# Performance work log

Hardware: AMD Instinct MI355X
Metric: run time of the kernel (lower is better)

The kernel has to match this reference:

```python
import jax, jax.numpy as jnp
import numpy as np

B, T = 32, 1024
VOCAB, E, H, K = 50000, 256, 512, 48
HD = H // 2
NEG = -10000.0


def setup_inputs() -> dict:
    key = jax.random.key(0)
    ks = jax.random.split(key, 8)
    n = lambda k, sh, sc: jax.random.normal(k, sh, jnp.float32) * sc
    return {
        "sentence": jax.random.randint(ks[0], (B, T), 0, VOCAB, dtype=jnp.int32),
        "embedding": n(ks[1], (VOCAB, E), 0.02),
        "Wih_f": n(ks[2], (4 * HD, E), 0.05), "Whh_f": n(ks[3], (4 * HD, HD), 0.05),
        "bih_f": jnp.zeros((4 * HD,), jnp.float32), "bhh_f": jnp.zeros((4 * HD,), jnp.float32),
        "Wih_b": n(ks[4], (4 * HD, E), 0.05), "Whh_b": n(ks[5], (4 * HD, HD), 0.05),
        "bih_b": jnp.zeros((4 * HD,), jnp.float32), "bhh_b": jnp.zeros((4 * HD,), jnp.float32),
        "W_out": n(ks[6], (K, H), 0.05), "b_out": jnp.zeros((K,), jnp.float32),
        "transitions": n(ks[7], (K, K), 1.0),
    }


def _lstm_dir(x, Wih, Whh, bih, bhh, reverse):
    # x: [T,B,E]; PyTorch gate order i,f,g,o
    h0 = jnp.zeros((x.shape[1], Whh.shape[1]), x.dtype)

    def step(carry, xt):
        h, c = carry
        g = xt @ Wih.T + bih + h @ Whh.T + bhh
        i, f, gg, o = jnp.split(g, 4, axis=-1)
        c = jax.nn.sigmoid(f) * c + jax.nn.sigmoid(i) * jnp.tanh(gg)
        h = jax.nn.sigmoid(o) * jnp.tanh(c)
        return (h, c), h

    _, hs = jax.lax.scan(step, (h0, h0), x, reverse=reverse)
    return hs  # [T,B,HD]


def _feats(sentence, embedding, Wih_f, Whh_f, bih_f, bhh_f,
           Wih_b, Whh_b, bih_b, bhh_b, W_out, b_out):
    x = jnp.swapaxes(embedding[sentence], 0, 1)  # [T,B,E]
    hf = _lstm_dir(x, Wih_f, Whh_f, bih_f, bhh_f, False)
    hb = _lstm_dir(x, Wih_b, Whh_b, bih_b, bhh_b, True)
    h = jnp.concatenate([hf, hb], axis=-1)       # [T,B,H]
    return jnp.swapaxes(h @ W_out.T + b_out, 0, 1)  # [B,T,K]


def _viterbi(feats, transitions):
    Bn, Tn, Kn = feats.shape
    ar = jnp.arange(Bn)
    fv0 = jnp.full((Bn, Kn), NEG, feats.dtype).at[:, Kn - 1].set(0.0)

    def step(fv, feat_t):
        # ntv[b, next, prev] = fv[b, prev] + transitions[next, prev]
        ntv = fv[:, None, :] + transitions[None, :, :]
        bptr = jnp.argmax(ntv, axis=2)               # [B,K]
        fv_new = jnp.max(ntv, axis=2) + feat_t       # [B,K]
        return fv_new, bptr

    fv, bptrs = jax.lax.scan(step, fv0, jnp.swapaxes(feats, 0, 1))  # bptrs: [T,B,K]
    last = jnp.argmax(fv, axis=1)

    def back(tag, bptr_t):
        return bptr_t[ar, tag], tag

    _, tags = jax.lax.scan(back, last, bptrs, reverse=True)  # [T,B], tags[t] = best tag at time t
    tag_seq = jnp.swapaxes(tags, 0, 1)  # [B,T]

    # NOTE: faithfully replicates the original code, which scores tag_seq[:,0]
    # with the FINAL timestep's emission (loop variable `feat` after the loop).
    feat_last = feats[:, -1, :]
    score = feat_last[ar, tag_seq[:, 0]]
    score = score + jnp.sum(transitions[tag_seq[:, :-1], tag_seq[:, 1:]], axis=1)
    score = score + jnp.sum(
        jnp.take_along_axis(feats[:, 1:, :], tag_seq[:, 1:, None], axis=2)[..., 0], axis=1)
    return score, tag_seq


def reference(sentence, embedding, Wih_f, Whh_f, bih_f, bhh_f,
              Wih_b, Whh_b, bih_b, bhh_b, W_out, b_out, transitions):
    feats = _feats(sentence, embedding, Wih_f, Whh_f, bih_f, bhh_f,
                   Wih_b, Whh_b, bih_b, bhh_b, W_out, b_out)
    return _viterbi(feats, transitions)
```

## Files before the change

kernel.cpp:

```cpp
#include <hip/hip_runtime.h>
#include <hip/hip_bf16.h>
#include <stdint.h>

typedef __attribute__((ext_vector_type(4))) float f32x4;
typedef __attribute__((ext_vector_type(4))) int   i32x4;
typedef __attribute__((ext_vector_type(8))) short short8;
typedef unsigned long long u64;

#define B_   32
#define T_   1024
#define E_   256
#define HD_  256
#define K_   48
#define NEG_ (-10000.0f)
#define SMAX 1056

__device__ __forceinline__ short f2bf(float f){
  union { float f; unsigned u; } v; v.f = f;
  unsigned r = v.u + 0x7fffu + ((v.u >> 16) & 1u);
  return (short)(r >> 16);
}
__device__ __forceinline__ short8 pack8v(float4 a, float4 b){
  short8 r;
  r[0]=f2bf(a.x); r[1]=f2bf(a.y); r[2]=f2bf(a.z); r[3]=f2bf(a.w);
  r[4]=f2bf(b.x); r[5]=f2bf(b.y); r[6]=f2bf(b.z); r[7]=f2bf(b.w);
  return r;
}
__device__ __forceinline__ float sigm(float x){ return 1.0f/(1.0f + __expf(-x)); }
__device__ __forceinline__ float tanh_f(float x){ return 1.0f - 2.0f/(1.0f + __expf(2.0f*x)); }

__global__ __launch_bounds__(128, 1)
void lstm_k(const int* __restrict__ sent, const float* __restrict__ emb,
            const float* __restrict__ Wih_f, const float* __restrict__ Whh_f,
            const float* __restrict__ bih_f, const float* __restrict__ bhh_f,
            const float* __restrict__ Wih_b, const float* __restrict__ Whh_b,
            const float* __restrict__ bih_b, const float* __restrict__ bhh_b,
            unsigned short* __restrict__ h_ex, unsigned* __restrict__ flags,
            unsigned short* __restrict__ h_all)
{
  __shared__ __align__(16) unsigned short WihLds[64*256];
  __shared__ __align__(16) unsigned short tile[32][16];

  const int bid  = blockIdx.x;
  const int dir  = bid & 1;
  const int w    = bid >> 1;
  const int tid  = threadIdx.x;
  const int wave = tid >> 6;
  const int lane = tid & 63;
  const int l15  = lane & 15;
  const int lq   = lane >> 4;

  const float* Wih = dir ? Wih_b : Wih_f;
  const float* Whh = dir ? Whh_b : Whh_f;
  const float* bih = dir ? bih_b : bih_f;
  const float* bhh = dir ? bhh_b : bhh_f;

  for (int idx = tid; idx < 64*256; idx += 128){
    int n = idx >> 8, kus = idx & 255;
    int j = (n >> 4)*256 + w*16 + (n & 15);
    WihLds[n*256 + (kus ^ ((n & 7) << 3))] = (unsigned short)f2bf(Wih[j*256 + kus]);
  }

  short8 wh[4][8];
  #pragma unroll
  for (int g = 0; g < 4; ++g){
    int j = g*256 + w*16 + l15;
    #pragma unroll
    for (int kc = 0; kc < 8; ++kc){
      const float* p = Whh + j*256 + kc*32 + lq*8;
      float4 a = *(const float4*)p, b = *(const float4*)(p + 4);
      wh[g][kc] = pack8v(a, b);
    }
  }
  float bias[4];
  #pragma unroll
  for (int g = 0; g < 4; ++g){
    int j = g*256 + w*16 + l15;
    bias[g] = bih[j] + bhh[j];
  }

  float c[4] = {0.f, 0.f, 0.f, 0.f};
  const int arow = wave*16 + l15;
  int tok = sent[arow*T_ + (dir ? (T_-1) : 0)];

  __syncthreads();

  for (int s = 0; s < T_; ++s){
    const int t_idx = dir ? (T_-1 - s) : s;

    const float* xr = emb + (long)tok*E_ + lq*8;
    float4 xa0[8], xa1[8];
    #pragma unroll
    for (int kc = 0; kc < 8; ++kc){
      xa0[kc] = *(const float4*)(xr + kc*32);
      xa1[kc] = *(const float4*)(xr + kc*32 + 4);
    }
    if (s + 1 < T_) tok = sent[arow*T_ + (dir ? (T_-2 - s) : (s+1))];

    f32x4 acc[4];
    #pragma unroll
    for (int g = 0; g < 4; ++g) acc[g] = (f32x4){bias[g], bias[g], bias[g], bias[g]};

    #pragma unroll
    for (int kc = 0; kc < 8; ++kc){
      short8 xa = pack8v(xa0[kc], xa1[kc]);
      #pragma unroll
      for (int g = 0; g < 4; ++g){
        int n = g*16 + l15;
        short8 bw = *(const short8*)&WihLds[n*256 + ((kc*32 + lq*8) ^ ((n & 7) << 3))];
        acc[g] = __builtin_amdgcn_mfma_f32_16x16x32_bf16(xa, bw, acc[g], 0, 0, 0);
      }
    }

    if (s > 0){
      const unsigned* fl = flags +
          ((((size_t)dir*SMAX + s)*2 + wave)*16 + l15)*4;
      for (;;){
        unsigned v = __hip_atomic_load(fl, __ATOMIC_RELAXED, __HIP_MEMORY_SCOPE_AGENT);
        if (__all(v != 0)) break;
      }

      const unsigned short* hb = h_ex + ((size_t)(s & 1)*2 + dir)*B_*HD_
                                 + (size_t)arow*HD_ + lq*8;
      i32x4 hv[8];
      #pragma unroll
      for (int kc = 0; kc < 8; ++kc)
        asm volatile("global_load_dwordx4 %0, %1, off sc0 sc1"
                     : "=v"(hv[kc]) : "v"(hb + kc*32));
      asm volatile("s_waitcnt vmcnt(0)" ::: "memory");
      __builtin_amdgcn_sched_barrier(0);

      #pragma unroll
      for (int kc = 0; kc < 8; ++kc){
        short8 ha = __builtin_bit_cast(short8, hv[kc]);
        #pragma unroll
        for (int g = 0; g < 4; ++g)
          acc[g] = __builtin_amdgcn_mfma_f32_16x16x32_bf16(ha, wh[g][kc], acc[g], 0, 0, 0);
      }
    }

    #pragma unroll
    for (int r = 0; r < 4; ++r){
      float iv = sigm(acc[0][r]);
      float fv = sigm(acc[1][r]);
      float gv = tanh_f(acc[2][r]);
      float ov = sigm(acc[3][r]);
      c[r] = fv*c[r] + iv*gv;
      float hv = ov*tanh_f(c[r]);
      tile[wave*16 + lq*4 + r][l15] = (unsigned short)f2bf(hv);
    }
    {
      int m2 = wave*16 + (lane >> 2);
      int u0 = (lane & 3)*4;
      u64 v = *(const u64*)&tile[m2][u0];
      size_t eoff = (size_t)m2*HD_ + w*16 + u0;
      u64* hw64 = (u64*)h_ex + ((size_t)((s+1) & 1)*2 + dir)*B_*(HD_/4) + eoff/4;
      __hip_atomic_store(hw64, v, __ATOMIC_RELAXED, __HIP_MEMORY_SCOPE_AGENT);
      u64* hs64 = (u64*)h_all + ((size_t)dir*T_ + t_idx)*B_*(HD_/4) + eoff/4;
      *hs64 = v;
    }

    asm volatile("s_waitcnt vmcnt(0)" ::: "memory");
    if (lane == 0)
      __hip_atomic_store(flags + ((((size_t)dir*SMAX + (s+1))*2 + wave)*16 + w)*4,
                         1u, __ATOMIC_RELAXED, __HIP_MEMORY_SCOPE_AGENT);
  }
}

__global__ __launch_bounds__(128)
void feats_k(const unsigned short* __restrict__ h_all,
             const float* __restrict__ W_out, const float* __restrict__ b_out,
             float* __restrict__ feats)
{
  __shared__ __align__(16) unsigned short Wlds[48*512];

  const int t0   = blockIdx.x * 4;
  const int tid  = threadIdx.x;
  const int wv   = tid >> 6;
  const int lane = tid & 63;
  const int l15  = lane & 15;
  const int lq   = lane >> 4;

  for (int idx = tid; idx < 48*512; idx += 128){
    int n = idx >> 9, kus = idx & 511;
    Wlds[n*512 + (kus ^ ((n & 7) << 3))] = (unsigned short)f2bf(W_out[n*512 + kus]);
  }
  float bo[3];
  #pragma unroll
  for (int nt = 0; nt < 3; ++nt) bo[nt] = b_out[nt*16 + l15];
  __syncthreads();

  #pragma unroll
  for (int mi = 0; mi < 4; ++mi){
    int mt = wv*4 + mi;
    int m  = mt*16 + l15;
    int b  = m & 31, tl = m >> 5;
    const unsigned short* hf = h_all + (size_t)((t0 + tl)*B_ + b)*HD_ + lq*8;
    const unsigned short* hb = h_all + (size_t)((T_ + t0 + tl)*B_ + b)*HD_ + lq*8;
    short8 af[16];
    #pragma unroll
    for (int kc = 0; kc < 8; ++kc) af[kc]     = *(const short8*)(hf + kc*32);
    #pragma unroll
    for (int kc = 0; kc < 8; ++kc) af[kc + 8] = *(const short8*)(hb + kc*32);

    f32x4 acc[3];
    #pragma unroll
    for (int nt = 0; nt < 3; ++nt) acc[nt] = (f32x4){bo[nt], bo[nt], bo[nt], bo[nt]};
    #pragma unroll
    for (int kc = 0; kc < 16; ++kc){
      #pragma unroll
      for (int nt = 0; nt < 3; ++nt){
        int n = nt*16 + l15;
        short8 bw = *(const short8*)&Wlds[n*512 + ((kc*32 + lq*8) ^ ((n & 7) << 3))];
        acc[nt] = __builtin_amdgcn_mfma_f32_16x16x32_bf16(af[kc], bw, acc[nt], 0, 0, 0);
      }
    }
    #pragma unroll
    for (int nt = 0; nt < 3; ++nt){
      #pragma unroll
      for (int r = 0; r < 4; ++r){
        int mm = mt*16 + lq*4 + r;
        int bb = mm & 31, tt = t0 + (mm >> 5);
        feats[(size_t)(bb*T_ + tt)*K_ + nt*16 + l15] = acc[nt][r];
      }
    }
  }
}

__global__ __launch_bounds__(64)
void viterbi_k(const float* __restrict__ feats, const float* __restrict__ trans,
               float* __restrict__ out)
{
  __shared__ float trans_s[K_*K_];
  __shared__ unsigned char bp[T_][K_];
  __shared__ unsigned char tags[T_];
  __shared__ float red[64];

  const int b = blockIdx.x, lane = threadIdx.x;
  for (int i = lane; i < K_*K_; i += 64) trans_s[i] = trans[i];

  float trow[K_];
  if (lane < K_){
    #pragma unroll
    for (int j = 0; j < K_; ++j) trow[j] = trans[lane*K_ + j];
  }
  float fv = (lane == K_-1) ? 0.0f : NEG_;
  const float* fb = feats + (size_t)b*T_*K_;
  __syncthreads();

  for (int t = 0; t < T_; ++t){
    float ft = (lane < K_) ? fb[t*K_ + lane] : 0.0f;
    float m = __shfl(fv, 0) + trow[0];
    int idx = 0;
    #pragma unroll
    for (int j = 1; j < K_; ++j){
      float v = __shfl(fv, j) + trow[j];
      if (v > m){ m = v; idx = j; }
    }
    if (lane < K_){
      fv = m + ft;
      bp[t][lane] = (unsigned char)idx;
    }
  }
  __syncthreads();

  red[lane] = fv;
  __syncthreads();
  int last = 0;
  {
    float bm = red[0];
    for (int k = 1; k < K_; ++k){ float v = red[k]; if (v > bm){ bm = v; last = k; } }
  }
  if (lane == 0){
    int tg = last;
    tags[T_-1] = (unsigned char)tg;
    for (int t = T_-1; t >= 1; --t){
      tg = bp[t][tg];
      tags[t-1] = (unsigned char)tg;
    }
  }
  __syncthreads();

  float sc = 0.0f;
  for (int t = 1 + lane; t < T_; t += 64){
    int tt = tags[t], tp = tags[t-1];
    sc += fb[t*K_ + tt] + trans_s[tp*K_ + tt];
  }
  if (lane == 0) sc += fb[(T_-1)*K_ + tags[0]];
  red[lane] = sc;
  __syncthreads();
  if (lane == 0){
    float tot = 0.f;
    for (int i = 0; i < 64; ++i) tot += red[i];
    out[b] = tot;
  }
  for (int t = lane; t < T_; t += 64)
    out[B_ + b*T_ + t] = (float)tags[t];
}

extern "C" void kernel_launch(void* const* d_in, const int* in_sizes, int n_in,
                              void* d_out, int out_size, void* d_ws, size_t ws_size,
                              hipStream_t stream)
{
  const int*   sent  = (const int*)  d_in[0];
  const float* emb   = (const float*)d_in[1];
  const float* Wih_f = (const float*)d_in[2];
  const float* Whh_f = (const float*)d_in[3];
  const float* bih_f = (const float*)d_in[4];
  const float* bhh_f = (const float*)d_in[5];
  const float* Wih_b = (const float*)d_in[6];
  const float* Whh_b = (const float*)d_in[7];
  const float* bih_b = (const float*)d_in[8];
  const float* bhh_b = (const float*)d_in[9];
  const float* W_out = (const float*)d_in[10];
  const float* b_out = (const float*)d_in[11];
  const float* trans = (const float*)d_in[12];

  char* ws = (char*)d_ws;
  unsigned short* h_ex  = (unsigned short*)ws;
  unsigned*       flags = (unsigned*)(ws + 65536);
  unsigned short* h_all = (unsigned short*)(ws + 2228224);
  float*          feats = (float*)(ws + 35782656);

  hipMemsetAsync(ws + 65536, 0, 2162688, stream);

  hipLaunchKernelGGL(lstm_k, dim3(32), dim3(128), 0, stream,
                     sent, emb, Wih_f, Whh_f, bih_f, bhh_f,
                     Wih_b, Whh_b, bih_b, bhh_b, h_ex, flags, h_all);
  hipLaunchKernelGGL(feats_k, dim3(256), dim3(128), 0, stream,
                     h_all, W_out, b_out, feats);
  hipLaunchKernelGGL(viterbi_k, dim3(32), dim3(64), 0, stream,
                     feats, trans, (float*)d_out);
}
```

Measured before the change: 4.556 ms.

## Replace flag-based LSTM step sync with sentinel-polled hidden states and pre-gathered bf16 inputs

Removes the per-step flag array and its separate store-then-flag handshake. h_all is prefilled with 0xFF sentinels and consumers poll the previous step's hidden state directly until no sentinel remains, which saves one round trip of global-memory latency per recurrent step. Embedding lookup and bf16 conversion move to a separate gather kernel so the recurrent loop only loads ready bf16 rows. It also prefetches the next emission in Viterbi. The costs are a 32MB memset, an extra kernel launch, and correctness that depends on no real bf16 pair equalling the 0xFFFF sentinel (a NaN pattern).

```diff
diff --git a/kernel.cpp b/kernel.cpp
--- a/kernel.cpp
+++ b/kernel.cpp
@@ -13,7 +13,6 @@
 #define HD_  256
 #define K_   48
 #define NEG_ (-10000.0f)
-#define SMAX 1056
 
 __device__ __forceinline__ short f2bf(float f){
   union { float f; unsigned u; } v; v.f = f;
@@ -29,13 +28,31 @@
 __device__ __forceinline__ float sigm(float x){ return 1.0f/(1.0f + __expf(-x)); }
 __device__ __forceinline__ float tanh_f(float x){ return 1.0f - 2.0f/(1.0f + __expf(2.0f*x)); }
 
+__global__ __launch_bounds__(256)
+void xgather_k(const int* __restrict__ sent, const float* __restrict__ emb,
+               unsigned short* __restrict__ xbf)
+{
+  const int t = blockIdx.x;
+  const int b = threadIdx.x >> 3;
+  const int e0 = (threadIdx.x & 7) * 4;
+  const int tok = sent[b*T_ + t];
+  const float* src = emb + (size_t)tok*E_;
+  unsigned short* dst = xbf + ((size_t)t*B_ + b)*E_;
+  #pragma unroll
+  for (int i = 0; i < 8; ++i){
+    float4 v = *(const float4*)(src + e0 + i*32);
+    union { unsigned short s[4]; u64 q; } u;
+    u.s[0]=f2bf(v.x); u.s[1]=f2bf(v.y); u.s[2]=f2bf(v.z); u.s[3]=f2bf(v.w);
+    *(u64*)(dst + e0 + i*32) = u.q;
+  }
+}
+
 __global__ __launch_bounds__(128, 1)
-void lstm_k(const int* __restrict__ sent, const float* __restrict__ emb,
-            const float* __restrict__ Wih_f, const float* __restrict__ Whh_f,
-            const float* __restrict__ bih_f, const float* __restrict__ bhh_f,
-            const float* __restrict__ Wih_b, const float* __restrict__ Whh_b,
+void lstm_k(const unsigned short* __restrict__ xbf,
+            const float* __restrict__ Whh_f, const float* __restrict__ bih_f,
+            const float* __restrict__ bhh_f, const float* __restrict__ Whh_b,
             const float* __restrict__ bih_b, const float* __restrict__ bhh_b,
-            unsigned short* __restrict__ h_ex, unsigned* __restrict__ flags,
+            const float* __restrict__ Wih_f, const float* __restrict__ Wih_b,
             unsigned short* __restrict__ h_all)
 {
   __shared__ __align__(16) unsigned short WihLds[64*256];
@@ -81,54 +98,49 @@
 
   float c[4] = {0.f, 0.f, 0.f, 0.f};
   const int arow = wave*16 + l15;
-  int tok = sent[arow*T_ + (dir ? (T_-1) : 0)];
 
   __syncthreads();
 
   for (int s = 0; s < T_; ++s){
-    const int t_idx = dir ? (T_-1 - s) : s;
-
-    const float* xr = emb + (long)tok*E_ + lq*8;
-    float4 xa0[8], xa1[8];
+    const int t_idx  = dir ? (T_-1 - s) : s;
+
+    const unsigned short* xr = xbf + ((size_t)t_idx*B_ + arow)*E_ + lq*8;
+    short8 xa[8];
+    #pragma unroll
+    for (int kc = 0; kc < 8; ++kc) xa[kc] = *(const short8*)(xr + kc*32);
+
+    f32x4 acc[4];
+    #pragma unroll
+    for (int g = 0; g < 4; ++g) acc[g] = (f32x4){bias[g], bias[g], bias[g], bias[g]};
+
     #pragma unroll
     for (int kc = 0; kc < 8; ++kc){
-      xa0[kc] = *(const float4*)(xr + kc*32);
-      xa1[kc] = *(const float4*)(xr + kc*32 + 4);
-    }
-    if (s + 1 < T_) tok = sent[arow*T_ + (dir ? (T_-2 - s) : (s+1))];
-
-    f32x4 acc[4];
-    #pragma unroll
-    for (int g = 0; g < 4; ++g) acc[g] = (f32x4){bias[g], bias[g], bias[g], bias[g]};
-
-    #pragma unroll
-    for (int kc = 0; kc < 8; ++kc){
-      short8 xa = pack8v(xa0[kc], xa1[kc]);
       #pragma unroll
       for (int g = 0; g < 4; ++g){
         int n = g*16 + l15;
         short8 bw = *(const short8*)&WihLds[n*256 + ((kc*32 + lq*8) ^ ((n & 7) << 3))];
-        acc[g] = __builtin_amdgcn_mfma_f32_16x16x32_bf16(xa, bw, acc[g], 0, 0, 0);
+        acc[g] = __builtin_amdgcn_mfma_f32_16x16x32_bf16(xa[kc], bw, acc[g], 0, 0, 0);
       }
     }
 
     if (s > 0){
-      const unsigned* fl = flags +
-          ((((size_t)dir*SMAX + s)*2 + wave)*16 + l15)*4;
-      for (;;){
-        unsigned v = __hip_atomic_load(fl, __ATOMIC_RELAXED, __HIP_MEMORY_SCOPE_AGENT);
-        if (__all(v != 0)) break;
-      }
-
-      const unsigned short* hb = h_ex + ((size_t)(s & 1)*2 + dir)*B_*HD_
+      const int t_prev = dir ? (T_ - s) : (s - 1);
+      const unsigned short* hb = h_all + ((size_t)dir*T_ + t_prev)*B_*HD_
                                  + (size_t)arow*HD_ + lq*8;
       i32x4 hv[8];
-      #pragma unroll
-      for (int kc = 0; kc < 8; ++kc)
-        asm volatile("global_load_dwordx4 %0, %1, off sc0 sc1"
-                     : "=v"(hv[kc]) : "v"(hb + kc*32));
-      asm volatile("s_waitcnt vmcnt(0)" ::: "memory");
-      __builtin_amdgcn_sched_barrier(0);
+      for (;;){
+        #pragma unroll
+        for (int kc = 0; kc < 8; ++kc)
+          asm volatile("global_load_dwordx4 %0, %1, off sc0 sc1"
+                       : "=&v"(hv[kc]) : "v"(hb + kc*32));
+        asm volatile("s_waitcnt vmcnt(0)" ::: "memory");
+        __builtin_amdgcn_sched_barrier(0);
+        int bad = 0;
+        #pragma unroll
+        for (int kc = 0; kc < 8; ++kc)
+          bad |= (hv[kc][0] == -1) | (hv[kc][2] == -1);
+        if (!__any(bad)) break;
+      }
 
       #pragma unroll
       for (int kc = 0; kc < 8; ++kc){
@@ -154,16 +166,9 @@
       int u0 = (lane & 3)*4;
       u64 v = *(const u64*)&tile[m2][u0];
       size_t eoff = (size_t)m2*HD_ + w*16 + u0;
-      u64* hw64 = (u64*)h_ex + ((size_t)((s+1) & 1)*2 + dir)*B_*(HD_/4) + eoff/4;
-      __hip_atomic_store(hw64, v, __ATOMIC_RELAXED, __HIP_MEMORY_SCOPE_AGENT);
       u64* hs64 = (u64*)h_all + ((size_t)dir*T_ + t_idx)*B_*(HD_/4) + eoff/4;
-      *hs64 = v;
-    }
-
-    asm volatile("s_waitcnt vmcnt(0)" ::: "memory");
-    if (lane == 0)
-      __hip_atomic_store(flags + ((((size_t)dir*SMAX + (s+1))*2 + wave)*16 + w)*4,
-                         1u, __ATOMIC_RELAXED, __HIP_MEMORY_SCOPE_AGENT);
+      __hip_atomic_store(hs64, v, __ATOMIC_RELAXED, __HIP_MEMORY_SCOPE_AGENT);
+    }
   }
 }
 
@@ -248,8 +253,9 @@
   const float* fb = feats + (size_t)b*T_*K_;
   __syncthreads();
 
+  float ft = (lane < K_) ? fb[lane] : 0.0f;
   for (int t = 0; t < T_; ++t){
-    float ft = (lane < K_) ? fb[t*K_ + lane] : 0.0f;
+    float ftn = (lane < K_ && t+1 < T_) ? fb[(t+1)*K_ + lane] : 0.0f;
     float m = __shfl(fv, 0) + trow[0];
     int idx = 0;
     #pragma unroll
@@ -261,6 +267,7 @@
       fv = m + ft;
       bp[t][lane] = (unsigned char)idx;
     }
+    ft = ftn;
   }
   __syncthreads();
 
@@ -317,16 +324,16 @@
   const float* trans = (const float*)d_in[12];
 
   char* ws = (char*)d_ws;
-  unsigned short* h_ex  = (unsigned short*)ws;
-  unsigned*       flags = (unsigned*)(ws + 65536);
-  unsigned short* h_all = (unsigned short*)(ws + 2228224);
-  float*          feats = (float*)(ws + 35782656);
-
-  hipMemsetAsync(ws + 65536, 0, 2162688, stream);
-
+  unsigned short* h_all = (unsigned short*)ws;
+  float*          feats = (float*)(ws + 33554432);
+  unsigned short* xbf   = (unsigned short*)(ws + 33554432 + 6291456);
+
+  hipMemsetAsync(h_all, 0xFF, 33554432, stream);
+
+  hipLaunchKernelGGL(xgather_k, dim3(T_), dim3(256), 0, stream, sent, emb, xbf);
   hipLaunchKernelGGL(lstm_k, dim3(32), dim3(128), 0, stream,
-                     sent, emb, Wih_f, Whh_f, bih_f, bhh_f,
-                     Wih_b, Whh_b, bih_b, bhh_b, h_ex, flags, h_all);
+                     xbf, Whh_f, bih_f, bhh_f, Whh_b, bih_b, bhh_b,
+                     Wih_f, Wih_b, h_all);
   hipLaunchKernelGGL(feats_k, dim3(256), dim3(128), 0, stream,
                      h_all, W_out, b_out, feats);
   hipLaunchKernelGGL(viterbi_k, dim3(32), dim3(64), 0, stream,
```

Measured after the change: 3.783 ms. -17.0%, faster.
